# Kernel optimization log

Measured on AMD Instinct MI355X. Metric: run time of the kernel, lower is better.

Reference implementation:

```python
import jax, jax.numpy as jnp
import numpy as np

B, N, C = 32, 197, 768   # batch, tokens (num_patches+1), emb_dim
KW = 197                 # kw_dim = seq_len
L = 12                   # num_layers (weights shared, norms per-layer)
HID = 3072               # mlp hidden = 4*emb_dim


def layer_norm(x, g, b, eps=1e-5):
    mu = jnp.mean(x, axis=-1, keepdims=True)
    var = jnp.var(x, axis=-1, keepdims=True)
    return (x - mu) * jax.lax.rsqrt(var + eps) * g + b


def attention(x, qkv_w, fc_w, fc_b, ln_g, ln_b, fc2_w, fc2_b, num_heads):
    b, n, c = x.shape
    d = c // num_heads
    qkv = (x @ qkv_w).reshape(b, n, 3, num_heads, d)
    q = qkv[:, :, 0].transpose(0, 2, 1, 3)  # [B,H,N,d]
    k = qkv[:, :, 1].transpose(0, 2, 1, 3)
    v = qkv[:, :, 2].transpose(0, 2, 1, 3)
    scale = d ** -0.5
    attn = jnp.einsum('bhnd,bhmd->bhnm', q, k) * scale      # [B,H,N,N]
    attn = attn @ fc_w + fc_b                                # [B,H,N,KW]
    attn = layer_norm(attn, ln_g, ln_b)
    attn = jax.nn.softmax(attn, axis=-1)
    attn = attn.transpose(0, 1, 3, 2)                        # [B,H,KW,N]
    y = jnp.einsum('bhkn,bhnd->bhkd', attn, v)               # [B,H,KW,d]
    # fc2 applied along KW axis of y.transpose(-2,-1): out[b,h,n,d]
    out = jnp.einsum('bhkd,kn->bnhd', y, fc2_w) + fc2_b[None, :, None, None]
    return out.reshape(b, n, c)


def mlp(x, w1, b1, w2, b2):
    return jax.nn.gelu(x @ w1 + b1, approximate=False) @ w2 + b2


def setup_inputs() -> dict:
    key = jax.random.key(0)
    ks = jax.random.split(key, 16)
    s = 0.02
    return {
        'x': jax.random.normal(ks[0], (B, N, C), jnp.float32),
        'qkv_w': jax.random.normal(ks[1], (C, 3 * C), jnp.float32) * s,
        'fc_w': jax.random.normal(ks[2], (N, KW), jnp.float32) * s,
        'fc_b': jnp.zeros((KW,), jnp.float32),
        'attn_ln_g': jnp.ones((KW,), jnp.float32),
        'attn_ln_b': jnp.zeros((KW,), jnp.float32),
        'fc2_w': jax.random.normal(ks[3], (KW, N), jnp.float32) * s,
        'fc2_b': jnp.zeros((N,), jnp.float32),
        'mlp_w1': jax.random.normal(ks[4], (C, HID), jnp.float32) * s,
        'mlp_b1': jnp.zeros((HID,), jnp.float32),
        'mlp_w2': jax.random.normal(ks[5], (HID, C), jnp.float32) * s,
        'mlp_b2': jnp.zeros((C,), jnp.float32),
        'f_ln_g': jnp.ones((L, C), jnp.float32),
        'f_ln_b': jnp.zeros((L, C), jnp.float32),
        'g_ln_g': jnp.ones((L, C), jnp.float32),
        'g_ln_b': jnp.zeros((L, C), jnp.float32),
        'num_heads': 12,
    }


def reference(x, qkv_w, fc_w, fc_b, attn_ln_g, attn_ln_b, fc2_w, fc2_b,
              mlp_w1, mlp_b1, mlp_w2, mlp_b2, f_ln_g, f_ln_b, g_ln_g, g_ln_b,
              num_heads):
    # x -> cat([x,x]) -> reversible stack -> mean of the two halves
    x1, x2 = x, x
    n_layers = f_ln_g.shape[0]
    for i in range(n_layers):
        # y1 = x1 + f(x2); y2 = x2 + g(y1)  (PreNorm wraps f and g)
        y1 = x1 + attention(layer_norm(x2, f_ln_g[i], f_ln_b[i]),
                            qkv_w, fc_w, fc_b, attn_ln_g, attn_ln_b,
                            fc2_w, fc2_b, num_heads)
        y2 = x2 + mlp(layer_norm(y1, g_ln_g[i], g_ln_b[i]),
                      mlp_w1, mlp_b1, mlp_w2, mlp_b2)
        x1, x2 = y1, y2
    return (x1 + x2) * 0.5
```

## Files before the change

### kernel.cpp

```cpp
#include <hip/hip_runtime.h>
#include <math.h>

#define BB   32
#define NN   197
#define CC   768
#define HH   12
#define DD   64
#define KWW  197
#define HIDD 3072
#define NL   12
#define RR   (BB*NN)
#define BHH  (BB*HH)
#define NP   224

typedef __attribute__((ext_vector_type(8))) short short8;
typedef __attribute__((ext_vector_type(4))) float floatx4;
typedef __attribute__((ext_vector_type(4))) unsigned short us4;

__device__ __forceinline__ unsigned short f2bf(float f) {
    unsigned int u = __float_as_uint(f);
    u += 0x7fff + ((u >> 16) & 1);
    return (unsigned short)(u >> 16);
}

__global__ void ln768_kernel(const float* __restrict__ in, const float* __restrict__ g,
                             const float* __restrict__ be, unsigned short* __restrict__ out) {
    int row = blockIdx.x;
    const float* x = in + (size_t)row * CC;
    unsigned short* o = out + (size_t)row * CC;
    int t = threadIdx.x;
    float v0 = x[t], v1 = x[t+256], v2 = x[t+512];
    float s = v0+v1+v2;
    float q = v0*v0+v1*v1+v2*v2;
    for (int off = 1; off < 64; off <<= 1) {
        s += __shfl_xor(s, off, 64);
        q += __shfl_xor(q, off, 64);
    }
    __shared__ float sh[8];
    int wv = t >> 6, ln = t & 63;
    if (ln == 0) { sh[wv] = s; sh[4+wv] = q; }
    __syncthreads();
    s = sh[0]+sh[1]+sh[2]+sh[3];
    q = sh[4]+sh[5]+sh[6]+sh[7];
    float mu  = s * (1.0f/CC);
    float var = q * (1.0f/CC) - mu*mu;
    float rs  = rsqrtf(var + 1e-5f);
    o[t]     = f2bf((v0-mu)*rs*g[t]     + be[t]);
    o[t+256] = f2bf((v1-mu)*rs*g[t+256] + be[t+256]);
    o[t+512] = f2bf((v2-mu)*rs*g[t+512] + be[t+512]);
}

__global__ void reduce_ln(float* __restrict__ x2, const float* __restrict__ part,
                          const float* __restrict__ b2,
                          const float* __restrict__ g, const float* __restrict__ be,
                          unsigned short* __restrict__ out, int do_ln) {
    int row = blockIdx.x;
    float* xp = x2 + (size_t)row * CC;
    const float* p0 = part + (size_t)row * CC;
    const float* p1 = part + (size_t)RR*CC + (size_t)row * CC;
    int t = threadIdx.x;
    float v0 = xp[t]     + p0[t]     + p1[t]     + b2[t];
    float v1 = xp[t+256] + p0[t+256] + p1[t+256] + b2[t+256];
    float v2 = xp[t+512] + p0[t+512] + p1[t+512] + b2[t+512];
    xp[t] = v0; xp[t+256] = v1; xp[t+512] = v2;
    if (!do_ln) return;
    float s = v0+v1+v2;
    float q = v0*v0+v1*v1+v2*v2;
    for (int off = 1; off < 64; off <<= 1) {
        s += __shfl_xor(s, off, 64);
        q += __shfl_xor(q, off, 64);
    }
    __shared__ float sh[8];
    int wv = t >> 6, ln = t & 63;
    if (ln == 0) { sh[wv] = s; sh[4+wv] = q; }
    __syncthreads();
    s = sh[0]+sh[1]+sh[2]+sh[3];
    q = sh[4]+sh[5]+sh[6]+sh[7];
    float mu  = s * (1.0f/CC);
    float var = q * (1.0f/CC) - mu*mu;
    float rs  = rsqrtf(var + 1e-5f);
    unsigned short* o = out + (size_t)row * CC;
    o[t]     = f2bf((v0-mu)*rs*g[t]     + be[t]);
    o[t+256] = f2bf((v1-mu)*rs*g[t+256] + be[t+256]);
    o[t+512] = f2bf((v2-mu)*rs*g[t+512] + be[t+512]);
}

__global__ void transpose_cast(const float* __restrict__ in, unsigned short* __restrict__ out,
                               int K, int Nd, int Kpad) {
    __shared__ float tile[32][33];
    int n0 = blockIdx.x*32, k0 = blockIdx.y*32;
    int tx = threadIdx.x & 31, ty = threadIdx.x >> 5;
    #pragma unroll
    for (int i = 0; i < 4; i++) {
        int k = k0 + ty + i*8;
        tile[ty + i*8][tx] = (k < K && n0+tx < Nd) ? in[(size_t)k*Nd + n0 + tx] : 0.f;
    }
    __syncthreads();
    #pragma unroll
    for (int i = 0; i < 4; i++) {
        int n = n0 + ty + i*8;
        if (n < Nd && k0 + tx < Kpad) out[(size_t)n*Kpad + k0 + tx] = f2bf(tile[tx][ty + i*8]);
    }
}

template<int BM, int BN, int WM, int WN, int WGN, int EPI, int KS>
__global__ __launch_bounds__(256) void gemm_bf16(
    const unsigned short* __restrict__ A, const unsigned short* __restrict__ Bt,
    const float* __restrict__ bias, float* __restrict__ Cf, unsigned short* __restrict__ Cb,
    int M, int Nd, int K)
{
    __shared__ unsigned short As[BM*32];
    __shared__ unsigned short Bs[BN*32];
    int tid  = threadIdx.x;
    int wv   = tid >> 6, lane = tid & 63;
    int wm   = wv / WGN, wn = wv % WGN;
    int bm   = blockIdx.y * BM, bn = blockIdx.x * BN;
    int quad = lane >> 4, mrow = lane & 15;
    int srow = lane >> 2;
    int skof = (lane & 3) * 8;
    floatx4 acc[WM][WN];
    #pragma unroll
    for (int i = 0; i < WM; i++)
        #pragma unroll
        for (int j = 0; j < WN; j++) acc[i][j] = (floatx4){0.f,0.f,0.f,0.f};

    const int Kc = K / KS;
    const int kbase = (KS > 1) ? blockIdx.z * Kc : 0;
    for (int k0 = kbase; k0 < kbase + Kc; k0 += 32) {
        #pragma unroll
        for (int i = 0; i < BM/64; i++) {
            int r  = wv*(BM/4) + i*16 + srow;
            int gr = bm + r; if (gr > M-1) gr = M-1;
            __builtin_amdgcn_global_load_lds(
                (const __attribute__((address_space(1))) void*)(A + (size_t)gr*K + k0 + skof),
                (__attribute__((address_space(3))) void*)(As + (wv*(BM/4) + i*16)*32),
                16, 0, 0);
        }
        #pragma unroll
        for (int i = 0; i < BN/64; i++) {
            int r  = wv*(BN/4) + i*16 + srow;
            int gr = bn + r; if (gr > Nd-1) gr = Nd-1;
            __builtin_amdgcn_global_load_lds(
                (const __attribute__((address_space(1))) void*)(Bt + (size_t)gr*K + k0 + skof),
                (__attribute__((address_space(3))) void*)(Bs + (wv*(BN/4) + i*16)*32),
                16, 0, 0);
        }
        __syncthreads();
        short8 af[WM], bf[WN];
        #pragma unroll
        for (int mi = 0; mi < WM; mi++)
            af[mi] = *(const short8*)&As[(wm*WM*16 + mi*16 + mrow)*32 + quad*8];
        #pragma unroll
        for (int ni = 0; ni < WN; ni++)
            bf[ni] = *(const short8*)&Bs[(wn*WN*16 + ni*16 + mrow)*32 + quad*8];
        #pragma unroll
        for (int mi = 0; mi < WM; mi++)
            #pragma unroll
            for (int ni = 0; ni < WN; ni++)
                acc[mi][ni] = __builtin_amdgcn_mfma_f32_16x16x32_bf16(af[mi], bf[ni], acc[mi][ni], 0, 0, 0);
        __syncthreads();
    }

    float* Cfz = (EPI == 5) ? (Cf + (size_t)blockIdx.z * M * Nd) : Cf;
    #pragma unroll
    for (int mi = 0; mi < WM; mi++) {
        int row0 = bm + wm*WM*16 + mi*16 + quad*4;
        #pragma unroll
        for (int ni = 0; ni < WN; ni++) {
            int col = bn + wn*WN*16 + ni*16 + mrow;
            float bv = (EPI == 2) ? bias[col] : 0.f;
            #pragma unroll
            for (int r = 0; r < 4; r++) {
                int row = row0 + r;
                if (row >= M) continue;
                float v = acc[mi][ni][r] + bv;
                if (EPI == 2) {
                    v = v / (1.0f + __expf(-1.5957691216f*v*(1.0f + 0.044715f*v*v)));
                    Cb[(size_t)row*Nd + col] = f2bf(v);
                } else if (EPI == 5) {
                    Cfz[(size_t)row*Nd + col] = v;
                } else if (EPI == 4) {
                    int sel = col / CC;
                    int rem = col - sel*CC;
                    int h = rem >> 6, d = rem & 63;
                    int b = row / NN, n = row - b*NN;
                    int bh = b*HH + h;
                    unsigned short val = f2bf(v);
                    if (sel < 2)
                        Cb[((size_t)sel*BHH + bh)*NN*DD + (size_t)n*DD + d] = val;
                    else
                        Cb[(size_t)2*BHH*NN*DD + (size_t)bh*DD*NP + (size_t)d*NP + n] = val;
                } else {
                    Cf[(size_t)row*Nd + col] = v;
                }
            }
        }
    }
}

__global__ __launch_bounds__(256) void attn_score(
    const unsigned short* __restrict__ qb,
    const unsigned short* __restrict__ kb,
    const unsigned short* __restrict__ fw,
    const float* __restrict__ fbias,
    const float* __restrict__ g, const float* __restrict__ be,
    unsigned short* __restrict__ PT)
{
    int bh = blockIdx.y;
    int bm = blockIdx.x * 64;
    __shared__ unsigned short Ks[224*DD];
    __shared__ unsigned short S1s[64*NP];
    __shared__ unsigned short Bs[224*32];
    __shared__ float gls[NP], bls[NP], bbs[NP];
    int tid = threadIdx.x;
    if (tid < NP) {
        bool vc = tid < KWW;
        gls[tid] = vc ? g[tid]     : 1.f;
        bls[tid] = vc ? be[tid]    : 0.f;
        bbs[tid] = vc ? fbias[tid] : 0.f;
    }
    int wv = tid >> 6, lane = tid & 63;
    int quad = lane >> 4, mrow = lane & 15;

    {
        int lrow = lane >> 3, lko = (lane & 7) * 8;
        #pragma unroll
        for (int i = 0; i < 7; i++) {
            int r = wv*56 + i*8 + lrow;
            __builtin_amdgcn_global_load_lds(
                (const __attribute__((address_space(1))) void*)(kb + ((size_t)bh*NN + r)*DD + lko),
                (__attribute__((address_space(3))) void*)(Ks + (size_t)(wv*56 + i*8)*DD),
                16, 0, 0);
        }
    }
    int qrow = bm + wv*16 + mrow; if (qrow > NN-1) qrow = NN-1;
    short8 aq0 = *(const short8*)&qb[((size_t)bh*NN + qrow)*DD + quad*8];
    short8 aq1 = *(const short8*)&qb[((size_t)bh*NN + qrow)*DD + 32 + quad*8];
    __syncthreads();

    #pragma unroll
    for (int ni = 0; ni < 14; ni++) {
        floatx4 a = (floatx4){0.f,0.f,0.f,0.f};
        short8 bf0 = *(const short8*)&Ks[(size_t)(ni*16 + mrow)*DD + quad*8];
        short8 bf1 = *(const short8*)&Ks[(size_t)(ni*16 + mrow)*DD + 32 + quad*8];
        a = __builtin_amdgcn_mfma_f32_16x16x32_bf16(aq0, bf0, a, 0, 0, 0);
        a = __builtin_amdgcn_mfma_f32_16x16x32_bf16(aq1, bf1, a, 0, 0, 0);
        #pragma unroll
        for (int r = 0; r < 4; r++)
            S1s[(size_t)(wv*16 + quad*4 + r)*NP + ni*16 + mrow] = f2bf(a[r]*0.125f);
    }
    __syncthreads();

    floatx4 acc[14];
    #pragma unroll
    for (int j = 0; j < 14; j++) acc[j] = (floatx4){0.f,0.f,0.f,0.f};
    for (int k0 = 0; k0 < 7; k0++) {
        for (int c = wv; c < 14; c += 4) {
            int gr = c*16 + (lane >> 2); if (gr > KWW-1) gr = KWW-1;
            __builtin_amdgcn_global_load_lds(
                (const __attribute__((address_space(1))) void*)(fw + (size_t)gr*NP + k0*32 + (lane & 3)*8),
                (__attribute__((address_space(3))) void*)(Bs + (size_t)(c*16)*32),
                16, 0, 0);
        }
        __syncthreads();
        short8 af = *(const short8*)&S1s[(size_t)(wv*16 + mrow)*NP + k0*32 + quad*8];
        #pragma unroll
        for (int ni = 0; ni < 14; ni++) {
            short8 bf = *(const short8*)&Bs[(size_t)(ni*16 + mrow)*32 + quad*8];
            acc[ni] = __builtin_amdgcn_mfma_f32_16x16x32_bf16(af, bf, acc[ni], 0, 0, 0);
        }
        __syncthreads();
    }

    float s[4] = {}, q[4] = {};
    #pragma unroll
    for (int ni = 0; ni < 14; ni++) {
        int col = ni*16 + mrow;
        float cm = (col < KWW) ? 1.f : 0.f;
        #pragma unroll
        for (int r = 0; r < 4; r++) {
            float x = acc[ni][r] + bbs[col];
            acc[ni][r] = x;
            s[r] += x*cm; q[r] += x*x*cm;
        }
    }
    #pragma unroll
    for (int o = 1; o < 16; o <<= 1)
        #pragma unroll
        for (int r = 0; r < 4; r++) {
            s[r] += __shfl_xor(s[r], o, 64);
            q[r] += __shfl_xor(q[r], o, 64);
        }
    float mu[4], rs[4], mx[4];
    #pragma unroll
    for (int r = 0; r < 4; r++) {
        mu[r] = s[r] * (1.0f/KWW);
        float var = q[r] * (1.0f/KWW) - mu[r]*mu[r];
        rs[r] = rsqrtf(var + 1e-5f);
        mx[r] = -1e30f;
    }
    #pragma unroll
    for (int ni = 0; ni < 14; ni++) {
        int col = ni*16 + mrow;
        bool vc = col < KWW;
        #pragma unroll
        for (int r = 0; r < 4; r++) {
            float x = (acc[ni][r] - mu[r]) * rs[r] * gls[col] + bls[col];
            acc[ni][r] = x;
            if (vc) mx[r] = fmaxf(mx[r], x);
        }
    }
    #pragma unroll
    for (int o = 1; o < 16; o <<= 1)
        #pragma unroll
        for (int r = 0; r < 4; r++)
            mx[r] = fmaxf(mx[r], __shfl_xor(mx[r], o, 64));
    float se[4] = {};
    #pragma unroll
    for (int ni = 0; ni < 14; ni++) {
        int col = ni*16 + mrow;
        float cm = (col < KWW) ? 1.f : 0.f;
        #pragma unroll
        for (int r = 0; r < 4; r++) {
            float p = __expf(acc[ni][r] - mx[r]) * cm;
            acc[ni][r] = p;
            se[r] += p;
        }
    }
    #pragma unroll
    for (int o = 1; o < 16; o <<= 1)
        #pragma unroll
        for (int r = 0; r < 4; r++)
            se[r] += __shfl_xor(se[r], o, 64);
    unsigned short* Pb = PT + (size_t)bh*NP*NP;
    int row0 = bm + wv*16 + quad*4;
    float inv0 = 1.0f/se[0], inv1 = 1.0f/se[1], inv2 = 1.0f/se[2], inv3 = 1.0f/se[3];
    #pragma unroll
    for (int ni = 0; ni < 14; ni++) {
        int col = ni*16 + mrow;
        if (col >= KWW) continue;
        if (row0 + 3 < NN) {
            us4 o = { f2bf(acc[ni][0]*inv0), f2bf(acc[ni][1]*inv1),
                      f2bf(acc[ni][2]*inv2), f2bf(acc[ni][3]*inv3) };
            *(us4*)&Pb[(size_t)col*NP + row0] = o;
        } else {
            float invs[4] = {inv0, inv1, inv2, inv3};
            #pragma unroll
            for (int r = 0; r < 4; r++)
                if (row0 + r < NN)
                    Pb[(size_t)col*NP + row0 + r] = f2bf(acc[ni][r]*invs[r]);
        }
    }
}

__global__ __launch_bounds__(256) void attn_out2(
    const unsigned short* __restrict__ PT,
    const unsigned short* __restrict__ vT,
    const unsigned short* __restrict__ fw,
    const float* __restrict__ bias,
    float* __restrict__ x1)
{
    int dt = blockIdx.x;
    int bh = blockIdx.y; int b = bh / HH, h = bh - b*HH;
    __shared__ unsigned short yT[16*232];
    int wv = threadIdx.x >> 6, lane = threadIdx.x & 63;
    int quad = lane >> 4, mrow = lane & 15;
    const unsigned short* Pb = PT + (size_t)bh*NP*NP;
    const unsigned short* Vb = vT + (size_t)bh*DD*NP + (size_t)(dt*16)*NP;

    short8 bfv[7];
    #pragma unroll
    for (int kc = 0; kc < 7; kc++)
        bfv[kc] = *(const short8*)&Vb[(size_t)mrow*NP + kc*32 + quad*8];
    for (int t = wv; t < 14; t += 4) {
        floatx4 acc = (floatx4){0.f,0.f,0.f,0.f};
        #pragma unroll
        for (int kc = 0; kc < 7; kc++) {
            short8 af = *(const short8*)&Pb[(size_t)(t*16 + mrow)*NP + kc*32 + quad*8];
            acc = __builtin_amdgcn_mfma_f32_16x16x32_bf16(af, bfv[kc], acc, 0, 0, 0);
        }
        us4 o = { f2bf(acc[0]), f2bf(acc[1]), f2bf(acc[2]), f2bf(acc[3]) };
        *(us4*)&yT[mrow*232 + t*16 + quad*4] = o;
    }
    __syncthreads();

    short8 yf[7];
    #pragma unroll
    for (int kc = 0; kc < 7; kc++)
        yf[kc] = *(const short8*)&yT[mrow*232 + kc*32 + quad*8];
    float* xb = x1 + (size_t)b*NN*CC + (size_t)h*DD + dt*16 + mrow;
    for (int nt = wv; nt < 13; nt += 4) {
        floatx4 acc = (floatx4){0.f,0.f,0.f,0.f};
        #pragma unroll
        for (int kc = 0; kc < 7; kc++) {
            short8 af = *(const short8*)&fw[(size_t)(nt*16 + mrow)*NP + kc*32 + quad*8];
            acc = __builtin_amdgcn_mfma_f32_16x16x32_bf16(af, yf[kc], acc, 0, 0, 0);
        }
        #pragma unroll
        for (int r = 0; r < 4; r++) {
            int n = nt*16 + quad*4 + r;
            if (n < NN) xb[(size_t)n*CC] += acc[r] + bias[n];
        }
    }
}

__global__ void init_kernel(const float* __restrict__ x, float* __restrict__ x1,
                            float* __restrict__ x2, int n) {
    int i = blockIdx.x*256 + threadIdx.x;
    if (i < n) { float v = x[i]; x1[i] = v; x2[i] = v; }
}
__global__ void final_kernel(const float* __restrict__ x1, const float* __restrict__ x2,
                             float* __restrict__ o, int n) {
    int i = blockIdx.x*256 + threadIdx.x;
    if (i < n) o[i] = 0.5f*(x1[i]+x2[i]);
}

extern "C" void kernel_launch(void* const* d_in, const int* in_sizes, int n_in,
                              void* d_out, int out_size, void* d_ws, size_t ws_size,
                              hipStream_t stream) {
    const float* x     = (const float*)d_in[0];
    const float* qkv_w = (const float*)d_in[1];
    const float* fc_w  = (const float*)d_in[2];
    const float* fc_b  = (const float*)d_in[3];
    const float* alng  = (const float*)d_in[4];
    const float* alnb  = (const float*)d_in[5];
    const float* fc2w  = (const float*)d_in[6];
    const float* fc2b  = (const float*)d_in[7];
    const float* w1    = (const float*)d_in[8];
    const float* b1    = (const float*)d_in[9];
    const float* w2    = (const float*)d_in[10];
    const float* b2    = (const float*)d_in[11];
    const float* flng  = (const float*)d_in[12];
    const float* flnb  = (const float*)d_in[13];
    const float* glng  = (const float*)d_in[14];
    const float* glnb  = (const float*)d_in[15];
    float* out = (float*)d_out;

    float* ws = (float*)d_ws;
    size_t off = 0;
    float* x1 = ws + off; off += (size_t)RR*CC;
    float* x2 = ws + off; off += (size_t)RR*CC;
    float* part = ws + off; off += (size_t)2*RR*CC;
    unsigned short* lnb = (unsigned short*)(ws + off); off += (size_t)RR*CC/2;
    unsigned short* qkvo = (unsigned short*)(ws + off);
    unsigned short* qb = qkvo;
    unsigned short* kb = qkvo + (size_t)BHH*NN*DD;
    unsigned short* vT = qkvo + (size_t)2*BHH*NN*DD;
    off += ((size_t)2*BHH*NN*DD + (size_t)BHH*DD*NP + 1) / 2;
    unsigned short* PT   = (unsigned short*)(ws + off); off += (size_t)BHH*NP*NP/2;
    unsigned short* hid  = (unsigned short*)(ws + off); off += (size_t)RR*HIDD/2;
    unsigned short* qkv_wt = (unsigned short*)(ws + off); off += (size_t)3*CC*CC/2;
    unsigned short* w1t    = (unsigned short*)(ws + off); off += (size_t)CC*HIDD/2;
    unsigned short* w2t    = (unsigned short*)(ws + off); off += (size_t)CC*HIDD/2;
    unsigned short* fc_wt  = (unsigned short*)(ws + off); off += (size_t)NN*NP/2 + 16;
    unsigned short* fc2_wt = (unsigned short*)(ws + off); off += (size_t)NP*NP/2 + 16;

    hipMemsetAsync(vT, 0, (size_t)BHH*DD*NP*2, stream);
    hipMemsetAsync(fc2_wt, 0, (size_t)NP*NP*2, stream);

    transpose_cast<<<dim3(72, 24), 256, 0, stream>>>(qkv_w, qkv_wt, CC, 3*CC, CC);
    transpose_cast<<<dim3(96, 24), 256, 0, stream>>>(w1, w1t, CC, HIDD, CC);
    transpose_cast<<<dim3(24, 96), 256, 0, stream>>>(w2, w2t, HIDD, CC, HIDD);
    transpose_cast<<<dim3(7, 7),   256, 0, stream>>>(fc_w,  fc_wt,  NN, KWW, NP);
    transpose_cast<<<dim3(7, 7),   256, 0, stream>>>(fc2w,  fc2_wt, KWW, NN, NP);

    const int nel = RR*CC;
    init_kernel<<<(nel+255)/256, 256, 0, stream>>>(x, x1, x2, nel);

    const int MT = (RR + 127) / 128;
    ln768_kernel<<<RR, 256, 0, stream>>>(x2, flng, flnb, lnb);
    for (int l = 0; l < NL; l++) {
        gemm_bf16<128,128,4,4,2,4,1><<<dim3(3*CC/128, MT), 256, 0, stream>>>(
            lnb, qkv_wt, nullptr, nullptr, qb, RR, 3*CC, CC);
        attn_score<<<dim3(4, BHH), 256, 0, stream>>>(
            qb, kb, fc_wt, fc_b, alng, alnb, PT);
        attn_out2<<<dim3(4, BHH), 256, 0, stream>>>(PT, vT, fc2_wt, fc2b, x1);
        ln768_kernel<<<RR, 256, 0, stream>>>(x1, glng + l*CC, glnb + l*CC, lnb);
        gemm_bf16<128,128,4,4,2,2,1><<<dim3(HIDD/128, MT), 256, 0, stream>>>(
            lnb, w1t, b1, nullptr, hid, RR, HIDD, CC);
        gemm_bf16<128,64,2,4,1,5,2><<<dim3(CC/64, MT, 2), 256, 0, stream>>>(
            hid, w2t, nullptr, part, nullptr, RR, CC, HIDD);
        reduce_ln<<<RR, 256, 0, stream>>>(
            x2, part, b2, flng + ((l+1 < NL) ? (l+1)*CC : 0),
            flnb + ((l+1 < NL) ? (l+1)*CC : 0), lnb, (l+1 < NL) ? 1 : 0);
    }
    final_kernel<<<(nel+255)/256, 256, 0, stream>>>(x1, x2, out, nel);
}
```

Before: 3.747 ms.

## Read K and fc weights directly from global, pair tiles in attn_out, widen fc2 GEMM tile

attn_score no longer stages K and the fc weight tile through LDS with global_load_lds and barriers; each lane reads its MFMA operands straight from global memory, which frees LDS and removes seven barrier pairs. attn_out2 processes two row tiles per wave iteration so the MFMA chains of the two tiles can interleave. The MLP down-projection GEMM switches from a 128x64 to a 128x128 tile, halving the grid width. The direct global reads give up reuse of K and fc weights across the block's waves and rely on cache hits instead, and the larger tile may lower occupancy.

After: 3.952 ms. +5.5%, slower.

```diff
diff --git a/kernel.cpp b/kernel.cpp
--- a/kernel.cpp
+++ b/kernel.cpp
@@ -208,9 +208,7 @@
 {
     int bh = blockIdx.y;
     int bm = blockIdx.x * 64;
-    __shared__ unsigned short Ks[224*DD];
     __shared__ unsigned short S1s[64*NP];
-    __shared__ unsigned short Bs[224*32];
     __shared__ float gls[NP], bls[NP], bbs[NP];
     int tid = threadIdx.x;
     if (tid < NP) {
@@ -221,28 +219,18 @@
     }
     int wv = tid >> 6, lane = tid & 63;
     int quad = lane >> 4, mrow = lane & 15;
-
-    {
-        int lrow = lane >> 3, lko = (lane & 7) * 8;
-        #pragma unroll
-        for (int i = 0; i < 7; i++) {
-            int r = wv*56 + i*8 + lrow;
-            __builtin_amdgcn_global_load_lds(
-                (const __attribute__((address_space(1))) void*)(kb + ((size_t)bh*NN + r)*DD + lko),
-                (__attribute__((address_space(3))) void*)(Ks + (size_t)(wv*56 + i*8)*DD),
-                16, 0, 0);
-        }
-    }
+    const unsigned short* Kb = kb + (size_t)bh*NN*DD;
+
     int qrow = bm + wv*16 + mrow; if (qrow > NN-1) qrow = NN-1;
     short8 aq0 = *(const short8*)&qb[((size_t)bh*NN + qrow)*DD + quad*8];
     short8 aq1 = *(const short8*)&qb[((size_t)bh*NN + qrow)*DD + 32 + quad*8];
-    __syncthreads();
 
     #pragma unroll
     for (int ni = 0; ni < 14; ni++) {
+        int kr = ni*16 + mrow; if (kr > NN-1) kr = NN-1;
+        short8 bf0 = *(const short8*)&Kb[(size_t)kr*DD + quad*8];
+        short8 bf1 = *(const short8*)&Kb[(size_t)kr*DD + 32 + quad*8];
         floatx4 a = (floatx4){0.f,0.f,0.f,0.f};
-        short8 bf0 = *(const short8*)&Ks[(size_t)(ni*16 + mrow)*DD + quad*8];
-        short8 bf1 = *(const short8*)&Ks[(size_t)(ni*16 + mrow)*DD + 32 + quad*8];
         a = __builtin_amdgcn_mfma_f32_16x16x32_bf16(aq0, bf0, a, 0, 0, 0);
         a = __builtin_amdgcn_mfma_f32_16x16x32_bf16(aq1, bf1, a, 0, 0, 0);
         #pragma unroll
@@ -254,22 +242,15 @@
     floatx4 acc[14];
     #pragma unroll
     for (int j = 0; j < 14; j++) acc[j] = (floatx4){0.f,0.f,0.f,0.f};
+    #pragma unroll
     for (int k0 = 0; k0 < 7; k0++) {
-        for (int c = wv; c < 14; c += 4) {
-            int gr = c*16 + (lane >> 2); if (gr > KWW-1) gr = KWW-1;
-            __builtin_amdgcn_global_load_lds(
-                (const __attribute__((address_space(1))) void*)(fw + (size_t)gr*NP + k0*32 + (lane & 3)*8),
-                (__attribute__((address_space(3))) void*)(Bs + (size_t)(c*16)*32),
-                16, 0, 0);
-        }
-        __syncthreads();
         short8 af = *(const short8*)&S1s[(size_t)(wv*16 + mrow)*NP + k0*32 + quad*8];
         #pragma unroll
         for (int ni = 0; ni < 14; ni++) {
-            short8 bf = *(const short8*)&Bs[(size_t)(ni*16 + mrow)*32 + quad*8];
+            int fr = ni*16 + mrow; if (fr > KWW-1) fr = KWW-1;
+            short8 bf = *(const short8*)&fw[(size_t)fr*NP + k0*32 + quad*8];
             acc[ni] = __builtin_amdgcn_mfma_f32_16x16x32_bf16(af, bf, acc[ni], 0, 0, 0);
         }
-        __syncthreads();
     }
 
     float s[4] = {}, q[4] = {};
@@ -372,15 +353,27 @@
     #pragma unroll
     for (int kc = 0; kc < 7; kc++)
         bfv[kc] = *(const short8*)&Vb[(size_t)mrow*NP + kc*32 + quad*8];
-    for (int t = wv; t < 14; t += 4) {
-        floatx4 acc = (floatx4){0.f,0.f,0.f,0.f};
+    #pragma unroll
+    for (int i = 0; i < 2; i++) {
+        int t0 = wv + i*8, t1 = t0 + 4;
+        bool v1 = t1 < 14;
+        floatx4 a0 = (floatx4){0.f,0.f,0.f,0.f};
+        floatx4 a1 = (floatx4){0.f,0.f,0.f,0.f};
         #pragma unroll
         for (int kc = 0; kc < 7; kc++) {
-            short8 af = *(const short8*)&Pb[(size_t)(t*16 + mrow)*NP + kc*32 + quad*8];
-            acc = __builtin_amdgcn_mfma_f32_16x16x32_bf16(af, bfv[kc], acc, 0, 0, 0);
-        }
-        us4 o = { f2bf(acc[0]), f2bf(acc[1]), f2bf(acc[2]), f2bf(acc[3]) };
-        *(us4*)&yT[mrow*232 + t*16 + quad*4] = o;
+            short8 p0 = *(const short8*)&Pb[(size_t)(t0*16 + mrow)*NP + kc*32 + quad*8];
+            a0 = __builtin_amdgcn_mfma_f32_16x16x32_bf16(p0, bfv[kc], a0, 0, 0, 0);
+            if (v1) {
+                short8 p1 = *(const short8*)&Pb[(size_t)(t1*16 + mrow)*NP + kc*32 + quad*8];
+                a1 = __builtin_amdgcn_mfma_f32_16x16x32_bf16(p1, bfv[kc], a1, 0, 0, 0);
+            }
+        }
+        us4 o0 = { f2bf(a0[0]), f2bf(a0[1]), f2bf(a0[2]), f2bf(a0[3]) };
+        *(us4*)&yT[mrow*232 + t0*16 + quad*4] = o0;
+        if (v1) {
+            us4 o1 = { f2bf(a1[0]), f2bf(a1[1]), f2bf(a1[2]), f2bf(a1[3]) };
+            *(us4*)&yT[mrow*232 + t1*16 + quad*4] = o1;
+        }
     }
     __syncthreads();
 
@@ -389,17 +382,32 @@
     for (int kc = 0; kc < 7; kc++)
         yf[kc] = *(const short8*)&yT[mrow*232 + kc*32 + quad*8];
     float* xb = x1 + (size_t)b*NN*CC + (size_t)h*DD + dt*16 + mrow;
-    for (int nt = wv; nt < 13; nt += 4) {
-        floatx4 acc = (floatx4){0.f,0.f,0.f,0.f};
+    #pragma unroll
+    for (int i = 0; i < 2; i++) {
+        int n0t = wv + i*8, n1t = n0t + 4;
+        bool v1 = n1t < 13;
+        floatx4 a0 = (floatx4){0.f,0.f,0.f,0.f};
+        floatx4 a1 = (floatx4){0.f,0.f,0.f,0.f};
         #pragma unroll
         for (int kc = 0; kc < 7; kc++) {
-            short8 af = *(const short8*)&fw[(size_t)(nt*16 + mrow)*NP + kc*32 + quad*8];
-            acc = __builtin_amdgcn_mfma_f32_16x16x32_bf16(af, yf[kc], acc, 0, 0, 0);
+            short8 f0 = *(const short8*)&fw[(size_t)(n0t*16 + mrow)*NP + kc*32 + quad*8];
+            a0 = __builtin_amdgcn_mfma_f32_16x16x32_bf16(f0, yf[kc], a0, 0, 0, 0);
+            if (v1) {
+                short8 f1 = *(const short8*)&fw[(size_t)(n1t*16 + mrow)*NP + kc*32 + quad*8];
+                a1 = __builtin_amdgcn_mfma_f32_16x16x32_bf16(f1, yf[kc], a1, 0, 0, 0);
+            }
         }
         #pragma unroll
         for (int r = 0; r < 4; r++) {
-            int n = nt*16 + quad*4 + r;
-            if (n < NN) xb[(size_t)n*CC] += acc[r] + bias[n];
+            int n = n0t*16 + quad*4 + r;
+            if (n < NN) xb[(size_t)n*CC] += a0[r] + bias[n];
+        }
+        if (v1) {
+            #pragma unroll
+            for (int r = 0; r < 4; r++) {
+                int n = n1t*16 + quad*4 + r;
+                if (n < NN) xb[(size_t)n*CC] += a1[r] + bias[n];
+            }
         }
     }
 }
@@ -478,7 +486,7 @@
         ln768_kernel<<<RR, 256, 0, stream>>>(x1, glng + l*CC, glnb + l*CC, lnb);
         gemm_bf16<128,128,4,4,2,2,1><<<dim3(HIDD/128, MT), 256, 0, stream>>>(
             lnb, w1t, b1, nullptr, hid, RR, HIDD, CC);
-        gemm_bf16<128,64,2,4,1,5,2><<<dim3(CC/64, MT, 2), 256, 0, stream>>>(
+        gemm_bf16<128,128,4,4,2,5,2><<<dim3(CC/128, MT, 2), 256, 0, stream>>>(
             hid, w2t, nullptr, part, nullptr, RR, CC, HIDD);
         reduce_ln<<<RR, 256, 0, stream>>>(
             x2, part, b2, flng + ((l+1 < NL) ? (l+1)*CC : 0),
```
